# Kernel tuning notes

Measured on AMD Instinct MI355X. Metric: run time of the kernel, lower is better.

## Reference

```python
import jax, jax.numpy as jnp
import numpy as np

B, L, D = 8, 4096, 256
H, C = 2, 128
DEG = 16  # incoming ring neighbors per node (excluding self loop)


def _build_edge_index():
    # Block-diagonal graph replicated per batch element, like _get_buffer.
    i = np.arange(L)
    offs = np.arange(1, DEG + 1)
    src_g = ((i[:, None] + offs[None, :]) % L).reshape(-1)   # [L*DEG]
    dst_g = np.repeat(i, DEG)                                 # [L*DEG]
    base = (np.arange(B) * L)[:, None]
    src = (src_g[None, :] + base).reshape(-1)
    dst = (dst_g[None, :] + base).reshape(-1)
    # PyG GATConv: remove_self_loops + add_self_loops -> exactly one self loop/node
    self_idx = np.arange(B * L)
    src = np.concatenate([src, self_idx])
    dst = np.concatenate([dst, self_idx])
    return jnp.asarray(np.stack([src, dst]), dtype=jnp.int32)  # [2, E]


def setup_inputs() -> dict:
    key = jax.random.key(0)
    k0, k1, k2, k3 = jax.random.split(key, 4)
    glorot = 1.0 / np.sqrt(D)
    return {
        "x": jax.random.normal(k0, (B, L, D), jnp.float32),
        "edge_index": _build_edge_index(),
        "W": jax.random.normal(k1, (D, H * C), jnp.float32) * glorot,
        "att_src": jax.random.normal(k2, (H, C), jnp.float32) * (1.0 / np.sqrt(C)),
        "att_dst": jax.random.normal(k3, (H, C), jnp.float32) * (1.0 / np.sqrt(C)),
        "bias": jnp.zeros((H * C,), jnp.float32),
    }


def reference(x, edge_index, W, att_src, att_dst, bias):
    b, l, d = x.shape
    n = b * l
    h_, c_ = att_src.shape
    xf = x.reshape(n, d)                                   # flatten batch of graphs
    res = xf
    h = (xf @ W).reshape(n, h_, c_)                        # [N,H,C] projected features
    a_src = jnp.einsum('nhc,hc->nh', h, att_src)           # per-node src logits
    a_dst = jnp.einsum('nhc,hc->nh', h, att_dst)
    s, t = edge_index[0], edge_index[1]
    alpha = jax.nn.leaky_relu(a_src[s] + a_dst[t], 0.2)    # [E,H]
    # softmax over incoming edges of each destination node
    amax = jax.ops.segment_max(alpha, t, num_segments=n)
    ex = jnp.exp(alpha - amax[t])
    denom = jax.ops.segment_sum(ex, t, num_segments=n)
    attn = ex / jnp.where(denom[t] > 0, denom[t], 1.0)     # [E,H]
    msg = h[s] * attn[:, :, None]                          # [E,H,C]
    out = jax.ops.segment_sum(msg, t, num_segments=n).reshape(n, h_ * c_) + bias
    out = jax.nn.relu(out) + res                           # relu + residual
    return out.reshape(b, l, h_ * c_)
```

## Files before the change

### kernel.cpp

```cpp
#include <hip/hip_runtime.h>

#define LL 4096
#define DD 256
#define TM 64
#define HALO 16
#define ROWS (TM + HALO)
#define NTH 512
#define APAD 40
#define HTS 104
#define WBS 104
#define ABUF_BYTES (ROWS * APAD * 2)

typedef float f32x4 __attribute__((ext_vector_type(4)));
typedef __bf16 bf16x8 __attribute__((ext_vector_type(8)));
typedef unsigned short us8 __attribute__((ext_vector_type(8)));
typedef unsigned short us4 __attribute__((ext_vector_type(4)));
typedef unsigned int u32x2 __attribute__((ext_vector_type(2)));

__device__ __forceinline__ unsigned short f2bf(float f) {
    union { float f; unsigned u; } v; v.f = f;
    unsigned r = v.u + 0x7fffu + ((v.u >> 16) & 1u);
    return (unsigned short)(r >> 16);
}

#define KBAR() do {                                         \
    asm volatile("s_waitcnt lgkmcnt(0)" ::: "memory");      \
    __builtin_amdgcn_s_barrier();                           \
} while (0)

__global__ void prep_w(const float* __restrict__ W, unsigned short* __restrict__ Wt) {
    int t = blockIdx.x * blockDim.x + threadIdx.x;
    int l = t & 63;
    int kk = (t >> 6) & 7;
    int ct = t >> 9;
    int col = (ct << 4) + (l & 15);
    int kbase = kk * 32 + ((l >> 4) << 3);
    us8 v;
    for (int j = 0; j < 8; ++j) v[j] = f2bf(W[(kbase + j) * 256 + col]);
    *reinterpret_cast<us8*>(Wt + t * 8) = v;
}

__global__ __launch_bounds__(NTH, 4) void gat_fused(
    const float* __restrict__ x, const unsigned short* __restrict__ Wt,
    const float* __restrict__ att_src, const float* __restrict__ att_dst,
    const float* __restrict__ bias, float* __restrict__ out)
{
    __shared__ unsigned short h_t[256][HTS];
    __shared__ float alog[ROWS][2][2];
    __shared__ __align__(16) unsigned char smem_u[2 * 64 * WBS * 2];
    unsigned short (*abuf0)[APAD] = reinterpret_cast<unsigned short(*)[APAD]>(smem_u);
    unsigned short (*abuf1)[APAD] = reinterpret_cast<unsigned short(*)[APAD]>(smem_u + ABUF_BYTES);
    unsigned short (*wband)[WBS]  = reinterpret_cast<unsigned short(*)[WBS]>(smem_u);

    const int tid  = threadIdx.x;
    const int lane = tid & 63;
    const int wv   = tid >> 6;
    const int lo   = lane & 15;
    const int hi   = lane >> 4;
    const int blk  = blockIdx.x;
    const int batch = blk >> 6;
    const int i0    = (blk & 63) * TM;
    const long xbase = (long)batch * (LL * DD);
    const int ct0 = wv * 2;
    const int hd  = wv >> 2;

    {
        int chan = tid >> 1, half = tid & 1;
        us8 z = {0, 0, 0, 0, 0, 0, 0, 0};
        *reinterpret_cast<us8*>(&h_t[chan][80 + half * 8]) = z;
        if (tid < 320) ((float*)alog)[tid] = 0.f;
    }

    f32x4 acc[5][2];
    for (int a = 0; a < 5; ++a)
        for (int b = 0; b < 2; ++b)
            acc[a][b] = (f32x4){0.f, 0.f, 0.f, 0.f};

    const int s0r = tid >> 3, s0k = (tid & 7) << 2;
    const int s1r = (tid + 512) >> 3, s1k = ((tid + 512) & 7) << 2;
    const float* xrow0 = x + xbase + (long)((i0 + s0r) & (LL - 1)) * DD + s0k;
    const float* xrow1 = x + xbase + (long)((i0 + s1r) & (LL - 1)) * DD + s1k;
    const unsigned short* wtb0 = Wt + (size_t)(ct0 * 8 * 64 + lane) * 8;
    const unsigned short* wtb1 = Wt + (size_t)((ct0 + 1) * 8 * 64 + lane) * 8;

    float4 cur0, cur1, nxt0, nxt1;
    us8 braw0, braw1, nbraw0, nbraw1;

    cur0 = *reinterpret_cast<const float4*>(xrow0);
    if (tid < 128) cur1 = *reinterpret_cast<const float4*>(xrow1);
    braw0 = *reinterpret_cast<const us8*>(wtb0);
    braw1 = *reinterpret_cast<const us8*>(wtb1);
    {
        us4 p;
        p[0] = f2bf(cur0.x); p[1] = f2bf(cur0.y); p[2] = f2bf(cur0.z); p[3] = f2bf(cur0.w);
        *reinterpret_cast<us4*>(&abuf0[s0r][s0k]) = p;
        if (tid < 128) {
            us4 q;
            q[0] = f2bf(cur1.x); q[1] = f2bf(cur1.y); q[2] = f2bf(cur1.z); q[3] = f2bf(cur1.w);
            *reinterpret_cast<us4*>(&abuf0[s1r][s1k]) = q;
        }
    }

#pragma unroll
    for (int kk = 0; kk < 8; ++kk) {
        unsigned short (*buf)[APAD]  = (kk & 1) ? abuf1 : abuf0;
        unsigned short (*nbuf)[APAD] = (kk & 1) ? abuf0 : abuf1;
        if (kk < 7) {
            nxt0 = *reinterpret_cast<const float4*>(xrow0 + (kk + 1) * 32);
            if (tid < 128) nxt1 = *reinterpret_cast<const float4*>(xrow1 + (kk + 1) * 32);
            nbraw0 = *reinterpret_cast<const us8*>(wtb0 + (size_t)(kk + 1) * 64 * 8);
            nbraw1 = *reinterpret_cast<const us8*>(wtb1 + (size_t)(kk + 1) * 64 * 8);
        }
        KBAR();

        bf16x8 bfrag0 = __builtin_bit_cast(bf16x8, braw0);
        bf16x8 bfrag1 = __builtin_bit_cast(bf16x8, braw1);
        for (int rt = 0; rt < 5; ++rt) {
            us8 araw = *reinterpret_cast<const us8*>(&buf[rt * 16 + lo][hi * 8]);
            bf16x8 afrag = __builtin_bit_cast(bf16x8, araw);
            acc[rt][0] = __builtin_amdgcn_mfma_f32_16x16x32_bf16(bfrag0, afrag, acc[rt][0], 0, 0, 0);
            acc[rt][1] = __builtin_amdgcn_mfma_f32_16x16x32_bf16(bfrag1, afrag, acc[rt][1], 0, 0, 0);
        }

        if (kk < 7) {
            us4 p;
            p[0] = f2bf(nxt0.x); p[1] = f2bf(nxt0.y); p[2] = f2bf(nxt0.z); p[3] = f2bf(nxt0.w);
            *reinterpret_cast<us4*>(&nbuf[s0r][s0k]) = p;
            if (tid < 128) {
                us4 q;
                q[0] = f2bf(nxt1.x); q[1] = f2bf(nxt1.y); q[2] = f2bf(nxt1.z); q[3] = f2bf(nxt1.w);
                *reinterpret_cast<us4*>(&nbuf[s1r][s1k]) = q;
            }
            braw0 = nbraw0;
            braw1 = nbraw1;
        }
    }

    {
        const float4 as0 = *reinterpret_cast<const float4*>(att_src + ct0 * 16 + hi * 4);
        const float4 as1 = *reinterpret_cast<const float4*>(att_src + (ct0 + 1) * 16 + hi * 4);
        const float4 ad0 = *reinterpret_cast<const float4*>(att_dst + ct0 * 16 + hi * 4);
        const float4 ad1 = *reinterpret_cast<const float4*>(att_dst + (ct0 + 1) * 16 + hi * 4);

        float ps[5], pd[5];
        for (int rt = 0; rt < 5; ++rt) {
            f32x4 a0 = acc[rt][0], a1 = acc[rt][1];
            ps[rt] = a0[0] * as0.x + a0[1] * as0.y + a0[2] * as0.z + a0[3] * as0.w
                   + a1[0] * as1.x + a1[1] * as1.y + a1[2] * as1.z + a1[3] * as1.w;
            pd[rt] = a0[0] * ad0.x + a0[1] * ad0.y + a0[2] * ad0.z + a0[3] * ad0.w
                   + a1[0] * ad1.x + a1[1] * ad1.y + a1[2] * ad1.z + a1[3] * ad1.w;
            int xrow = rt * 16 + lo;
            for (int j = 0; j < 4; ++j)
                h_t[ct0 * 16 + hi * 4 + j][xrow] = f2bf(a0[j]);
            for (int j = 0; j < 4; ++j)
                h_t[(ct0 + 1) * 16 + hi * 4 + j][xrow] = f2bf(a1[j]);
        }
        for (int rt = 0; rt < 5; ++rt) {
            ps[rt] += __shfl_xor(ps[rt], 16);
            ps[rt] += __shfl_xor(ps[rt], 32);
            pd[rt] += __shfl_xor(pd[rt], 16);
            pd[rt] += __shfl_xor(pd[rt], 32);
        }
        if (hi == 0) {
            for (int rt = 0; rt < 5; ++rt) {
                atomicAdd(&alog[rt * 16 + lo][hd][0], ps[rt]);
                atomicAdd(&alog[rt * 16 + lo][hd][1], pd[rt]);
            }
        }
    }

    float4 res[4][2];
    for (int rt = 0; rt < 4; ++rt)
        for (int c = 0; c < 2; ++c)
            res[rt][c] = *reinterpret_cast<const float4*>(
                x + xbase + (long)(i0 + rt * 16 + lo) * DD + (ct0 + c) * 16 + hi * 4);

    __syncthreads();

    if (tid < 128) {
        int r = tid >> 1, h2 = tid & 1;
        unsigned short* wrow = &wband[h2 * 64 + r][0];
        us8 z = {0, 0, 0, 0, 0, 0, 0, 0};
        for (int q = 0; q < 13; ++q) *reinterpret_cast<us8*>(wrow + q * 8) = z;
        float ad = alog[r][h2][1];
        float al[17];
        float mx = -1e30f;
        for (int k = 0; k < 17; ++k) {
            float s = (k < 16) ? alog[r + 1 + k][h2][0] : alog[r][h2][0];
            float v = s + ad;
            v = (v > 0.f) ? v : 0.2f * v;
            al[k] = v;
            mx = fmaxf(mx, v);
        }
        float sum = 0.f;
        for (int k = 0; k < 17; ++k) { al[k] = __expf(al[k] - mx); sum += al[k]; }
        float inv = 1.f / sum;
        wrow[r] = f2bf(al[16] * inv);
        for (int k = 0; k < 16; ++k) wrow[r + 1 + k] = f2bf(al[k] * inv);
    }
    __syncthreads();

    {
        f32x4 acc2[4][2];
        for (int a = 0; a < 4; ++a)
            for (int b = 0; b < 2; ++b)
                acc2[a][b] = (f32x4){0.f, 0.f, 0.f, 0.f};

        for (int kq = 0; kq < 3; ++kq) {
            bf16x8 bfr[4];
            for (int rt = 0; rt < 4; ++rt) {
                us8 raw = *reinterpret_cast<const us8*>(
                    &wband[hd * 64 + rt * 16 + lo][kq * 32 + hi * 8]);
                bfr[rt] = __builtin_bit_cast(bf16x8, raw);
            }
            for (int c = 0; c < 2; ++c) {
                us8 araw = *reinterpret_cast<const us8*>(
                    &h_t[(ct0 + c) * 16 + lo][kq * 32 + hi * 8]);
                bf16x8 afr = __builtin_bit_cast(bf16x8, araw);
                for (int rt = 0; rt < 4; ++rt)
                    acc2[rt][c] = __builtin_amdgcn_mfma_f32_16x16x32_bf16(afr, bfr[rt], acc2[rt][c], 0, 0, 0);
            }
        }

        const float4 b40 = *reinterpret_cast<const float4*>(bias + ct0 * 16 + hi * 4);
        const float4 b41 = *reinterpret_cast<const float4*>(bias + (ct0 + 1) * 16 + hi * 4);
        for (int rt = 0; rt < 4; ++rt)
            for (int c = 0; c < 2; ++c) {
                const float4 b4 = c ? b41 : b40;
                f32x4 s = acc2[rt][c];
                long g = xbase + (long)(i0 + rt * 16 + lo) * DD + (ct0 + c) * 16 + hi * 4;
                float4 o;
                o.x = fmaxf(s[0] + b4.x, 0.f) + res[rt][c].x;
                o.y = fmaxf(s[1] + b4.y, 0.f) + res[rt][c].y;
                o.z = fmaxf(s[2] + b4.z, 0.f) + res[rt][c].z;
                o.w = fmaxf(s[3] + b4.w, 0.f) + res[rt][c].w;
                *reinterpret_cast<float4*>(out + g) = o;
            }
    }
}

extern "C" void kernel_launch(void* const* d_in, const int* in_sizes, int n_in,
                              void* d_out, int out_size, void* d_ws, size_t ws_size,
                              hipStream_t stream) {
    const float* x       = (const float*)d_in[0];
    const float* W       = (const float*)d_in[2];
    const float* att_src = (const float*)d_in[3];
    const float* att_dst = (const float*)d_in[4];
    const float* bias    = (const float*)d_in[5];
    float* out           = (float*)d_out;
    unsigned short* Wt   = (unsigned short*)d_ws;

    hipLaunchKernelGGL(prep_w, dim3(128), dim3(64), 0, stream, W, Wt);
    hipLaunchKernelGGL(gat_fused, dim3(512), dim3(NTH), 0, stream,
                       x, Wt, att_src, att_dst, bias, out);
}
```

Baseline: 32.49 us.

## Halve row tile to 32 rows with 256-thread blocks and wider per-wave column tiles

Shrinks each block's row tile from 64 to 32 nodes (48 rows with the 16-row halo), halves threads per block and doubles the grid to 1024 blocks. Each wave now owns four 16-column tiles instead of two. The attention band matrix and the aggregation MFMA loop are resized to a single 32-wide k-slice per 16-row tile. W fragment loads move after the MFMAs instead of being prefetched ahead. The aim is finer-grained scheduling and lower LDS and register use per block. The cost is a larger share of redundant halo projection work (48 rows computed per 32 output rows) and less lead time for the W loads.

After: 30.07 us. -7.4%, faster.

```diff
diff --git a/kernel.cpp b/kernel.cpp
--- a/kernel.cpp
+++ b/kernel.cpp
@@ -2,20 +2,19 @@
 
 #define LL 4096
 #define DD 256
-#define TM 64
+#define TM 32
 #define HALO 16
 #define ROWS (TM + HALO)
-#define NTH 512
+#define NTH 256
 #define APAD 40
-#define HTS 104
-#define WBS 104
+#define HTS 56
+#define WBS 40
 #define ABUF_BYTES (ROWS * APAD * 2)
 
 typedef float f32x4 __attribute__((ext_vector_type(4)));
 typedef __bf16 bf16x8 __attribute__((ext_vector_type(8)));
 typedef unsigned short us8 __attribute__((ext_vector_type(8)));
 typedef unsigned short us4 __attribute__((ext_vector_type(4)));
-typedef unsigned int u32x2 __attribute__((ext_vector_type(2)));
 
 __device__ __forceinline__ unsigned short f2bf(float f) {
     union { float f; unsigned u; } v; v.f = f;
@@ -47,7 +46,7 @@
 {
     __shared__ unsigned short h_t[256][HTS];
     __shared__ float alog[ROWS][2][2];
-    __shared__ __align__(16) unsigned char smem_u[2 * 64 * WBS * 2];
+    __shared__ __align__(16) unsigned char smem_u[2 * ABUF_BYTES];
     unsigned short (*abuf0)[APAD] = reinterpret_cast<unsigned short(*)[APAD]>(smem_u);
     unsigned short (*abuf1)[APAD] = reinterpret_cast<unsigned short(*)[APAD]>(smem_u + ABUF_BYTES);
     unsigned short (*wband)[WBS]  = reinterpret_cast<unsigned short(*)[WBS]>(smem_u);
@@ -58,38 +57,37 @@
     const int lo   = lane & 15;
     const int hi   = lane >> 4;
     const int blk  = blockIdx.x;
-    const int batch = blk >> 6;
-    const int i0    = (blk & 63) * TM;
+    const int batch = blk >> 7;
+    const int i0    = (blk & 127) * TM;
     const long xbase = (long)batch * (LL * DD);
-    const int ct0 = wv * 2;
-    const int hd  = wv >> 2;
-
-    {
-        int chan = tid >> 1, half = tid & 1;
-        us8 z = {0, 0, 0, 0, 0, 0, 0, 0};
-        *reinterpret_cast<us8*>(&h_t[chan][80 + half * 8]) = z;
-        if (tid < 320) ((float*)alog)[tid] = 0.f;
-    }
-
-    f32x4 acc[5][2];
-    for (int a = 0; a < 5; ++a)
-        for (int b = 0; b < 2; ++b)
+    const int ct0 = wv * 4;
+    const int hd  = wv >> 1;
+
+    if (tid < 192) ((float*)alog)[tid] = 0.f;
+
+    f32x4 acc[3][4];
+    for (int a = 0; a < 3; ++a)
+        for (int b = 0; b < 4; ++b)
             acc[a][b] = (f32x4){0.f, 0.f, 0.f, 0.f};
 
     const int s0r = tid >> 3, s0k = (tid & 7) << 2;
-    const int s1r = (tid + 512) >> 3, s1k = ((tid + 512) & 7) << 2;
+    const int s1r = (tid + 256) >> 3, s1k = (tid & 7) << 2;
     const float* xrow0 = x + xbase + (long)((i0 + s0r) & (LL - 1)) * DD + s0k;
     const float* xrow1 = x + xbase + (long)((i0 + s1r) & (LL - 1)) * DD + s1k;
-    const unsigned short* wtb0 = Wt + (size_t)(ct0 * 8 * 64 + lane) * 8;
+    const unsigned short* wtb0 = Wt + (size_t)((ct0 + 0) * 8 * 64 + lane) * 8;
     const unsigned short* wtb1 = Wt + (size_t)((ct0 + 1) * 8 * 64 + lane) * 8;
+    const unsigned short* wtb2 = Wt + (size_t)((ct0 + 2) * 8 * 64 + lane) * 8;
+    const unsigned short* wtb3 = Wt + (size_t)((ct0 + 3) * 8 * 64 + lane) * 8;
 
     float4 cur0, cur1, nxt0, nxt1;
-    us8 braw0, braw1, nbraw0, nbraw1;
+    us8 braw0, braw1, braw2, braw3;
 
     cur0 = *reinterpret_cast<const float4*>(xrow0);
     if (tid < 128) cur1 = *reinterpret_cast<const float4*>(xrow1);
     braw0 = *reinterpret_cast<const us8*>(wtb0);
     braw1 = *reinterpret_cast<const us8*>(wtb1);
+    braw2 = *reinterpret_cast<const us8*>(wtb2);
+    braw3 = *reinterpret_cast<const us8*>(wtb3);
     {
         us4 p;
         p[0] = f2bf(cur0.x); p[1] = f2bf(cur0.y); p[2] = f2bf(cur0.z); p[3] = f2bf(cur0.w);
@@ -108,21 +106,27 @@
         if (kk < 7) {
             nxt0 = *reinterpret_cast<const float4*>(xrow0 + (kk + 1) * 32);
             if (tid < 128) nxt1 = *reinterpret_cast<const float4*>(xrow1 + (kk + 1) * 32);
-            nbraw0 = *reinterpret_cast<const us8*>(wtb0 + (size_t)(kk + 1) * 64 * 8);
-            nbraw1 = *reinterpret_cast<const us8*>(wtb1 + (size_t)(kk + 1) * 64 * 8);
         }
         KBAR();
 
-        bf16x8 bfrag0 = __builtin_bit_cast(bf16x8, braw0);
-        bf16x8 bfrag1 = __builtin_bit_cast(bf16x8, braw1);
-        for (int rt = 0; rt < 5; ++rt) {
+        bf16x8 bf0 = __builtin_bit_cast(bf16x8, braw0);
+        bf16x8 bf1 = __builtin_bit_cast(bf16x8, braw1);
+        bf16x8 bf2 = __builtin_bit_cast(bf16x8, braw2);
+        bf16x8 bf3 = __builtin_bit_cast(bf16x8, braw3);
+        for (int rt = 0; rt < 3; ++rt) {
             us8 araw = *reinterpret_cast<const us8*>(&buf[rt * 16 + lo][hi * 8]);
             bf16x8 afrag = __builtin_bit_cast(bf16x8, araw);
-            acc[rt][0] = __builtin_amdgcn_mfma_f32_16x16x32_bf16(bfrag0, afrag, acc[rt][0], 0, 0, 0);
-            acc[rt][1] = __builtin_amdgcn_mfma_f32_16x16x32_bf16(bfrag1, afrag, acc[rt][1], 0, 0, 0);
+            acc[rt][0] = __builtin_amdgcn_mfma_f32_16x16x32_bf16(bf0, afrag, acc[rt][0], 0, 0, 0);
+            acc[rt][1] = __builtin_amdgcn_mfma_f32_16x16x32_bf16(bf1, afrag, acc[rt][1], 0, 0, 0);
+            acc[rt][2] = __builtin_amdgcn_mfma_f32_16x16x32_bf16(bf2, afrag, acc[rt][2], 0, 0, 0);
+            acc[rt][3] = __builtin_amdgcn_mfma_f32_16x16x32_bf16(bf3, afrag, acc[rt][3], 0, 0, 0);
         }
 
         if (kk < 7) {
+            braw0 = *reinterpret_cast<const us8*>(wtb0 + (size_t)(kk + 1) * 512);
+            braw1 = *reinterpret_cast<const us8*>(wtb1 + (size_t)(kk + 1) * 512);
+            braw2 = *reinterpret_cast<const us8*>(wtb2 + (size_t)(kk + 1) * 512);
+            braw3 = *reinterpret_cast<const us8*>(wtb3 + (size_t)(kk + 1) * 512);
             us4 p;
             p[0] = f2bf(nxt0.x); p[1] = f2bf(nxt0.y); p[2] = f2bf(nxt0.z); p[3] = f2bf(nxt0.w);
             *reinterpret_cast<us4*>(&nbuf[s0r][s0k]) = p;
@@ -131,57 +135,56 @@
                 q[0] = f2bf(nxt1.x); q[1] = f2bf(nxt1.y); q[2] = f2bf(nxt1.z); q[3] = f2bf(nxt1.w);
                 *reinterpret_cast<us4*>(&nbuf[s1r][s1k]) = q;
             }
-            braw0 = nbraw0;
-            braw1 = nbraw1;
         }
     }
 
     {
-        const float4 as0 = *reinterpret_cast<const float4*>(att_src + ct0 * 16 + hi * 4);
-        const float4 as1 = *reinterpret_cast<const float4*>(att_src + (ct0 + 1) * 16 + hi * 4);
-        const float4 ad0 = *reinterpret_cast<const float4*>(att_dst + ct0 * 16 + hi * 4);
-        const float4 ad1 = *reinterpret_cast<const float4*>(att_dst + (ct0 + 1) * 16 + hi * 4);
-
-        float ps[5], pd[5];
-        for (int rt = 0; rt < 5; ++rt) {
-            f32x4 a0 = acc[rt][0], a1 = acc[rt][1];
-            ps[rt] = a0[0] * as0.x + a0[1] * as0.y + a0[2] * as0.z + a0[3] * as0.w
-                   + a1[0] * as1.x + a1[1] * as1.y + a1[2] * as1.z + a1[3] * as1.w;
-            pd[rt] = a0[0] * ad0.x + a0[1] * ad0.y + a0[2] * ad0.z + a0[3] * ad0.w
-                   + a1[0] * ad1.x + a1[1] * ad1.y + a1[2] * ad1.z + a1[3] * ad1.w;
+        float4 as[4], ad[4];
+#pragma unroll
+        for (int c = 0; c < 4; ++c) {
+            as[c] = *reinterpret_cast<const float4*>(att_src + (ct0 + c) * 16 + hi * 4);
+            ad[c] = *reinterpret_cast<const float4*>(att_dst + (ct0 + c) * 16 + hi * 4);
+        }
+        float ps[3], pd[3];
+        for (int rt = 0; rt < 3; ++rt) {
+            ps[rt] = 0.f; pd[rt] = 0.f;
             int xrow = rt * 16 + lo;
-            for (int j = 0; j < 4; ++j)
-                h_t[ct0 * 16 + hi * 4 + j][xrow] = f2bf(a0[j]);
-            for (int j = 0; j < 4; ++j)
-                h_t[(ct0 + 1) * 16 + hi * 4 + j][xrow] = f2bf(a1[j]);
-        }
-        for (int rt = 0; rt < 5; ++rt) {
+#pragma unroll
+            for (int c = 0; c < 4; ++c) {
+                f32x4 a = acc[rt][c];
+                ps[rt] += a[0] * as[c].x + a[1] * as[c].y + a[2] * as[c].z + a[3] * as[c].w;
+                pd[rt] += a[0] * ad[c].x + a[1] * ad[c].y + a[2] * ad[c].z + a[3] * ad[c].w;
+                for (int j = 0; j < 4; ++j)
+                    h_t[(ct0 + c) * 16 + hi * 4 + j][xrow] = f2bf(a[j]);
+            }
+        }
+        for (int rt = 0; rt < 3; ++rt) {
             ps[rt] += __shfl_xor(ps[rt], 16);
             ps[rt] += __shfl_xor(ps[rt], 32);
             pd[rt] += __shfl_xor(pd[rt], 16);
             pd[rt] += __shfl_xor(pd[rt], 32);
         }
         if (hi == 0) {
-            for (int rt = 0; rt < 5; ++rt) {
+            for (int rt = 0; rt < 3; ++rt) {
                 atomicAdd(&alog[rt * 16 + lo][hd][0], ps[rt]);
                 atomicAdd(&alog[rt * 16 + lo][hd][1], pd[rt]);
             }
         }
     }
 
-    float4 res[4][2];
-    for (int rt = 0; rt < 4; ++rt)
-        for (int c = 0; c < 2; ++c)
-            res[rt][c] = *reinterpret_cast<const float4*>(
-                x + xbase + (long)(i0 + rt * 16 + lo) * DD + (ct0 + c) * 16 + hi * 4);
+    float4 res[2][4];
+    for (int ti = 0; ti < 2; ++ti)
+        for (int c = 0; c < 4; ++c)
+            res[ti][c] = *reinterpret_cast<const float4*>(
+                x + xbase + (long)(i0 + ti * 16 + lo) * DD + (ct0 + c) * 16 + hi * 4);
 
     __syncthreads();
 
-    if (tid < 128) {
+    if (tid < 64) {
         int r = tid >> 1, h2 = tid & 1;
-        unsigned short* wrow = &wband[h2 * 64 + r][0];
+        unsigned short* wrow = &wband[h2 * 32 + r][0];
         us8 z = {0, 0, 0, 0, 0, 0, 0, 0};
-        for (int q = 0; q < 13; ++q) *reinterpret_cast<us8*>(wrow + q * 8) = z;
+        for (int q = 0; q < 5; ++q) *reinterpret_cast<us8*>(wrow + q * 8) = z;
         float ad = alog[r][h2][1];
         float al[17];
         float mx = -1e30f;
@@ -195,45 +198,41 @@
         float sum = 0.f;
         for (int k = 0; k < 17; ++k) { al[k] = __expf(al[k] - mx); sum += al[k]; }
         float inv = 1.f / sum;
-        wrow[r] = f2bf(al[16] * inv);
-        for (int k = 0; k < 16; ++k) wrow[r + 1 + k] = f2bf(al[k] * inv);
+        int lo_r = r & 15;
+        wrow[lo_r] = f2bf(al[16] * inv);
+        for (int k = 0; k < 16; ++k) wrow[lo_r + 1 + k] = f2bf(al[k] * inv);
     }
     __syncthreads();
 
     {
-        f32x4 acc2[4][2];
-        for (int a = 0; a < 4; ++a)
-            for (int b = 0; b < 2; ++b)
+        f32x4 acc2[2][4];
+        for (int a = 0; a < 2; ++a)
+            for (int b = 0; b < 4; ++b)
                 acc2[a][b] = (f32x4){0.f, 0.f, 0.f, 0.f};
 
-        for (int kq = 0; kq < 3; ++kq) {
-            bf16x8 bfr[4];
-            for (int rt = 0; rt < 4; ++rt) {
-                us8 raw = *reinterpret_cast<const us8*>(
-                    &wband[hd * 64 + rt * 16 + lo][kq * 32 + hi * 8]);
-                bfr[rt] = __builtin_bit_cast(bf16x8, raw);
-            }
-            for (int c = 0; c < 2; ++c) {
+        for (int ti = 0; ti < 2; ++ti) {
+            us8 raw = *reinterpret_cast<const us8*>(&wband[hd * 32 + ti * 16 + lo][hi * 8]);
+            bf16x8 bfr = __builtin_bit_cast(bf16x8, raw);
+#pragma unroll
+            for (int c = 0; c < 4; ++c) {
                 us8 araw = *reinterpret_cast<const us8*>(
-                    &h_t[(ct0 + c) * 16 + lo][kq * 32 + hi * 8]);
+                    &h_t[(ct0 + c) * 16 + lo][ti * 16 + hi * 8]);
                 bf16x8 afr = __builtin_bit_cast(bf16x8, araw);
-                for (int rt = 0; rt < 4; ++rt)
-                    acc2[rt][c] = __builtin_amdgcn_mfma_f32_16x16x32_bf16(afr, bfr[rt], acc2[rt][c], 0, 0, 0);
-            }
-        }
-
-        const float4 b40 = *reinterpret_cast<const float4*>(bias + ct0 * 16 + hi * 4);
-        const float4 b41 = *reinterpret_cast<const float4*>(bias + (ct0 + 1) * 16 + hi * 4);
-        for (int rt = 0; rt < 4; ++rt)
-            for (int c = 0; c < 2; ++c) {
-                const float4 b4 = c ? b41 : b40;
-                f32x4 s = acc2[rt][c];
-                long g = xbase + (long)(i0 + rt * 16 + lo) * DD + (ct0 + c) * 16 + hi * 4;
+                acc2[ti][c] = __builtin_amdgcn_mfma_f32_16x16x32_bf16(afr, bfr, acc2[ti][c], 0, 0, 0);
+            }
+        }
+
+        for (int ti = 0; ti < 2; ++ti)
+#pragma unroll
+            for (int c = 0; c < 4; ++c) {
+                const float4 b4 = *reinterpret_cast<const float4*>(bias + (ct0 + c) * 16 + hi * 4);
+                f32x4 s = acc2[ti][c];
+                long g = xbase + (long)(i0 + ti * 16 + lo) * DD + (ct0 + c) * 16 + hi * 4;
                 float4 o;
-                o.x = fmaxf(s[0] + b4.x, 0.f) + res[rt][c].x;
-                o.y = fmaxf(s[1] + b4.y, 0.f) + res[rt][c].y;
-                o.z = fmaxf(s[2] + b4.z, 0.f) + res[rt][c].z;
-                o.w = fmaxf(s[3] + b4.w, 0.f) + res[rt][c].w;
+                o.x = fmaxf(s[0] + b4.x, 0.f) + res[ti][c].x;
+                o.y = fmaxf(s[1] + b4.y, 0.f) + res[ti][c].y;
+                o.z = fmaxf(s[2] + b4.z, 0.f) + res[ti][c].z;
+                o.w = fmaxf(s[3] + b4.w, 0.f) + res[ti][c].w;
                 *reinterpret_cast<float4*>(out + g) = o;
             }
     }
@@ -251,6 +250,6 @@
     unsigned short* Wt   = (unsigned short*)d_ws;
 
     hipLaunchKernelGGL(prep_w, dim3(128), dim3(64), 0, stream, W, Wt);
-    hipLaunchKernelGGL(gat_fused, dim3(512), dim3(NTH), 0, stream,
+    hipLaunchKernelGGL(gat_fused, dim3(1024), dim3(NTH), 0, stream,
                        x, Wt, att_src, att_dst, bias, out);
 }
```
